# Kernel tuning notes

Measured on AMD Instinct MI355X. Metric: run time of the kernel, lower is better.

The kernel has to match this reference:

```python
import jax, jax.numpy as jnp
import numpy as np

BS = 4096
N_AGENTS = 8
INPUT_SHAPE = 256
H = 256
N_ACTIONS = 30


def setup_inputs() -> dict:
    key = jax.random.key(0)
    ks = jax.random.split(key, 10)
    return {
        "inputs": jax.random.normal(ks[0], (BS * N_AGENTS, INPUT_SHAPE), jnp.float32),
        "hidden_state": jax.random.normal(ks[1], (BS * N_AGENTS, H), jnp.float32),
        # hypernet-generated per-agent weights are relu outputs -> nonnegative
        "fc1_w": jax.random.uniform(ks[2], (N_AGENTS, INPUT_SHAPE, H), jnp.float32),
        "fc1_b": jax.random.uniform(ks[3], (N_AGENTS, H), jnp.float32),
        "rnn_ih_w": jax.random.uniform(ks[4], (N_AGENTS, H, 3 * H), jnp.float32),
        "rnn_ih_b": jax.random.uniform(ks[5], (N_AGENTS, 3 * H), jnp.float32),
        "rnn_hh_w": jax.random.uniform(ks[6], (N_AGENTS, H, 3 * H), jnp.float32),
        "rnn_hh_b": jax.random.uniform(ks[7], (N_AGENTS, 3 * H), jnp.float32),
        "fc2_w": jax.random.uniform(ks[8], (N_AGENTS, H, N_ACTIONS), jnp.float32),
        "fc2_b": jax.random.uniform(ks[9], (N_AGENTS, N_ACTIONS), jnp.float32),
    }


def reference(inputs, hidden_state, fc1_w, fc1_b, rnn_ih_w, rnn_ih_b,
              rnn_hh_w, rnn_hh_b, fc2_w, fc2_b):
    A = fc1_w.shape[0]
    inp = inputs.reshape(-1, A, fc1_w.shape[1])        # [bs, A, in]
    h_in = hidden_state.reshape(-1, A, rnn_hh_w.shape[1])  # [bs, A, H]

    # per-agent fc1: x = relu(inp @ fc1_w + fc1_b)
    x = jax.nn.relu(jnp.einsum('bai,aih->bah', inp, fc1_w) + fc1_b)

    # GRU-cell gate pre-activations with per-agent weights
    gi = jnp.einsum('bah,ahk->bak', x, rnn_ih_w) + rnn_ih_b     # [bs, A, 3H]
    gh = jnp.einsum('bah,ahk->bak', h_in, rnn_hh_w) + rnn_hh_b  # [bs, A, 3H]
    i_r, i_i, i_n = jnp.split(gi, 3, axis=-1)
    h_r, h_i, h_n = jnp.split(gh, 3, axis=-1)

    resetgate = jax.nn.sigmoid(i_r + h_r)
    inputgate = jax.nn.sigmoid(i_i + h_i)
    newgate = jnp.tanh(i_n + resetgate * h_n)
    h = newgate + inputgate * (h_in - newgate)          # [bs, A, H]

    q = jax.nn.relu(jnp.einsum('bah,aho->bao', h, fc2_w) + fc2_b)  # [bs, A, n_actions]
    return q.reshape(-1, q.shape[-1]), h.reshape(-1, h.shape[-1])
```

## Files before the change

### kernel.cpp

```cpp
#include <hip/hip_runtime.h>


typedef __attribute__((ext_vector_type(4))) float f32x4;
typedef __attribute__((ext_vector_type(8))) short s8;
typedef __attribute__((ext_vector_type(4))) unsigned short us4;
typedef __attribute__((ext_vector_type(8))) unsigned short us8;

#define QSIZE   983040
#define W1H_OFF 0
#define W1L_OFF 524288
#define WIH_OFF 1048576
#define WHH_OFF 2621440
#define W2T_OFF 4194304
#define XB_OFF  4259840
#define HB_OFF  12648448
#define RSX_U   21037056
#define RSH_U   21102592
#define WS_NEED_NEW 42336256ull

static __device__ __forceinline__ unsigned short f2bf(float f) {
  union { float f; unsigned u; } v; v.f = f;
  unsigned r = v.u + 0x7FFFu + ((v.u >> 16) & 1u);
  return (unsigned short)(r >> 16);
}
static __device__ __forceinline__ float bf2f(unsigned short u) {
  union { unsigned u; float f; } v; v.u = ((unsigned)u) << 16;
  return v.f;
}
static __device__ __forceinline__ float sigm(float x) {
  return 1.0f / (1.0f + __expf(-x));
}
static __device__ __forceinline__ float tanh_(float x) {
  return 1.0f - 2.0f / (__expf(2.0f * x) + 1.0f);
}

__global__ void prep_weights(const float* __restrict__ fc1w,
                             const float* __restrict__ rihw,
                             const float* __restrict__ rhhw,
                             const float* __restrict__ fc2w,
                             unsigned short* __restrict__ ws) {
  int q = blockIdx.x * 256 + threadIdx.x;
  if (q < 131072) {
    int a = q >> 14, rem = q & 16383;
    int cb = rem >> 10, s = rem & 1023;
    int ks = s >> 7, l4 = (s >> 5) & 3, l16 = (s >> 1) & 15, hf = s & 1;
    int n = cb * 16 + l16, k0 = ks * 32 + l4 * 8 + hf * 4;
    const float* sp = fc1w + a * 65536 + k0 * 256 + n;
    float v0 = sp[0], v1 = sp[256], v2 = sp[512], v3 = sp[768];
    us4 hi = { f2bf(v0), f2bf(v1), f2bf(v2), f2bf(v3) };
    us4 lo = { f2bf(v0 - bf2f(hi[0])), f2bf(v1 - bf2f(hi[1])),
               f2bf(v2 - bf2f(hi[2])), f2bf(v3 - bf2f(hi[3])) };
    int o = a * 65536 + cb * 4096 + ks * 512 + l4 * 128 + l16 * 8 + hf * 4;
    *(us4*)(ws + W1H_OFF + o) = hi;
    *(us4*)(ws + W1L_OFF + o) = lo;
  } else if (q < 524288) {
    int t = q - 131072;
    int a = t / 49152, rem = t % 49152;
    int cb = rem >> 10, s = rem & 1023;
    int ks = s >> 7, l4 = (s >> 5) & 3, l16 = (s >> 1) & 15, hf = s & 1;
    int n = cb * 16 + l16, k0 = ks * 32 + l4 * 8 + hf * 4;
    const float* sp = rihw + a * 196608 + k0 * 768 + n;
    us4 v = { f2bf(sp[0] - 0.5f), f2bf(sp[768] - 0.5f),
              f2bf(sp[1536] - 0.5f), f2bf(sp[2304] - 0.5f) };
    *(us4*)(ws + WIH_OFF + a * 196608 + cb * 4096 + ks * 512 + l4 * 128
            + l16 * 8 + hf * 4) = v;
  } else if (q < 917504) {
    int t = q - 524288;
    int a = t / 49152, rem = t % 49152;
    int cb = rem >> 10, s = rem & 1023;
    int ks = s >> 7, l4 = (s >> 5) & 3, l16 = (s >> 1) & 15, hf = s & 1;
    int n = cb * 16 + l16, k0 = ks * 32 + l4 * 8 + hf * 4;
    const float* sp = rhhw + a * 196608 + k0 * 768 + n;
    us4 v = { f2bf(sp[0] - 0.5f), f2bf(sp[768] - 0.5f),
              f2bf(sp[1536] - 0.5f), f2bf(sp[2304] - 0.5f) };
    *(us4*)(ws + WHH_OFF + a * 196608 + cb * 4096 + ks * 512 + l4 * 128
            + l16 * 8 + hf * 4) = v;
  } else if (q < 933888) {
    int t = q - 917504;
    int a = t >> 11, rem = t & 2047;
    int cb = rem >> 10, s = rem & 1023;
    int ks = s >> 7, l4 = (s >> 5) & 3, l16 = (s >> 1) & 15, hf = s & 1;
    int n = cb * 16 + l16, k0 = ks * 32 + l4 * 8 + hf * 4;
    us4 v = { 0, 0, 0, 0 };
    if (n < 30) {
      const float* sp = fc2w + a * 7680 + k0 * 30 + n;
      v = (us4){ f2bf(sp[0]), f2bf(sp[30]), f2bf(sp[60]), f2bf(sp[90]) };
    }
    *(us4*)(ws + W2T_OFF + a * 8192 + cb * 4096 + ks * 512 + l4 * 128
            + l16 * 8 + hf * 4) = v;
  }
}

static __device__ __forceinline__ void stage_split(unsigned short* p0,
                                                   unsigned short* p1,
                                                   const float* __restrict__ src,
                                                   int rowbase, int a, int tid) {
#pragma unroll
  for (int k = 0; k < 8; ++k) {
    int j = tid + k * 256;
    int r = j >> 6;
    int c4 = (j & 63) << 2;
    const float* p = src + ((((rowbase + r) << 3) + a) << 8) + c4;
    float4 v = *(const float4*)p;
    us4 hi = { f2bf(v.x), f2bf(v.y), f2bf(v.z), f2bf(v.w) };
    us4 lo = { f2bf(v.x - bf2f(hi[0])), f2bf(v.y - bf2f(hi[1])),
               f2bf(v.z - bf2f(hi[2])), f2bf(v.w - bf2f(hi[3])) };
    int idx = ((r << 8) + c4) ^ ((r & 7) << 3);
    *(us4*)(p0 + idx) = hi;
    *(us4*)(p1 + idx) = lo;
  }
}

static __device__ __forceinline__ void stage_single(unsigned short* p,
                                                    const float* __restrict__ src,
                                                    int rowbase, int a, int tid) {
#pragma unroll
  for (int k = 0; k < 8; ++k) {
    int j = tid + k * 256;
    int r = j >> 6;
    int c4 = (j & 63) << 2;
    const float* sp = src + ((((rowbase + r) << 3) + a) << 8) + c4;
    float4 v = *(const float4*)sp;
    us4 hi = { f2bf(v.x), f2bf(v.y), f2bf(v.z), f2bf(v.w) };
    int idx = ((r << 8) + c4) ^ ((r & 7) << 3);
    *(us4*)(p + idx) = hi;
  }
}

static __device__ __forceinline__ void mma64f(const unsigned short* lds,
                                              const unsigned short* __restrict__ wf,
                                              int cb0, int lane, int l16, int l4,
                                              f32x4 (&acc)[2][4]) {
#pragma unroll
  for (int ks = 0; ks < 8; ++ks) {
    s8 af[2], bw[4];
#pragma unroll
    for (int mt = 0; mt < 2; ++mt) {
      int row = mt * 16 + l16;
      int idx = ((row << 8) + ks * 32 + 8 * l4) ^ ((row & 7) << 3);
      af[mt] = *(const s8*)(lds + idx);
    }
#pragma unroll
    for (int nt = 0; nt < 4; ++nt)
      bw[nt] = *(const s8*)(wf + (cb0 + nt) * 4096 + ks * 512 + lane * 8);
#pragma unroll
    for (int mt = 0; mt < 2; ++mt)
#pragma unroll
      for (int nt = 0; nt < 4; ++nt)
        acc[mt][nt] = __builtin_amdgcn_mfma_f32_16x16x32_bf16(
            af[mt], bw[nt], acc[mt][nt], 0, 0, 0);
  }
}

static __device__ __forceinline__ void mma16f(const unsigned short* lds,
                                              const unsigned short* __restrict__ wf,
                                              int cb, int lane, int l16, int l4,
                                              f32x4 (&acc)[2]) {
#pragma unroll
  for (int ks = 0; ks < 8; ++ks) {
    s8 bw = *(const s8*)(wf + cb * 4096 + ks * 512 + lane * 8);
#pragma unroll
    for (int mt = 0; mt < 2; ++mt) {
      int row = mt * 16 + l16;
      int idx = ((row << 8) + ks * 32 + 8 * l4) ^ ((row & 7) << 3);
      s8 af = *(const s8*)(lds + idx);
      acc[mt] = __builtin_amdgcn_mfma_f32_16x16x32_bf16(af, bw, acc[mt], 0, 0, 0);
    }
  }
}

__global__ __launch_bounds__(256, 2) void k1_fc1(
    const float* __restrict__ inp, const float* __restrict__ hin,
    const float* __restrict__ b1, unsigned short* __restrict__ ws) {
  __shared__ __align__(16) unsigned short P0[32 * 256];
  __shared__ __align__(16) unsigned short P1[32 * 256];
  __shared__ float RSXP[8][32], RSHP[8][32];
  const int tid = threadIdx.x;
  const int a = blockIdx.x & 7;
  const int rt = blockIdx.x >> 3;
  const int rowbase = rt * 32;
  const int lane = tid & 63, w = tid >> 6;
  const int l16 = lane & 15, l4 = lane >> 4;
  const int n0 = w * 64;

  stage_split(P0, P1, inp, rowbase, a, tid);
  __syncthreads();

  f32x4 XA[2][4];
#pragma unroll
  for (int mt = 0; mt < 2; ++mt)
#pragma unroll
    for (int nt = 0; nt < 4; ++nt) XA[mt][nt] = (f32x4){0.f, 0.f, 0.f, 0.f};
  mma64f(P0, ws + W1H_OFF + a * 65536, w * 4, lane, l16, l4, XA);
  mma64f(P1, ws + W1H_OFF + a * 65536, w * 4, lane, l16, l4, XA);
  mma64f(P0, ws + W1L_OFF + a * 65536, w * 4, lane, l16, l4, XA);
  __syncthreads();

#pragma unroll
  for (int nt = 0; nt < 4; ++nt) {
    int col = n0 + nt * 16 + l16;
    float bb = b1[a * 256 + col];
#pragma unroll
    for (int mt = 0; mt < 2; ++mt)
#pragma unroll
      for (int r = 0; r < 4; ++r) {
        float v = fmaxf(XA[mt][nt][r] + bb, 0.f);
        int row = mt * 16 + l4 * 4 + r;
        P0[((row << 8) + col) ^ ((row & 7) << 3)] = f2bf(v);
      }
  }
  stage_single(P1, hin, rowbase, a, tid);
  __syncthreads();

  const int rbg = (a << 8) + rt * 2;
#pragma unroll
  for (int i = 0; i < 4; ++i) {
    int c = tid + i * 256;
    int rb = c >> 9, s = c & 511;
    int row = rb * 16 + (s & 15);
    int col = ((s >> 6) << 5) + (((s >> 4) & 3) << 3);
    int idx = ((row << 8) + col) ^ ((row & 7) << 3);
    *(us8*)(ws + XB_OFF + (rbg + rb) * 4096 + s * 8) = *(const us8*)(P0 + idx);
    *(us8*)(ws + HB_OFF + (rbg + rb) * 4096 + s * 8) = *(const us8*)(P1 + idx);
  }

  {
    int row = tid >> 3, qd = tid & 7;
    float sx = 0.f, sh = 0.f;
#pragma unroll
    for (int i = 0; i < 8; ++i) {
      int c = qd * 32 + i * 4;
      int idx = ((row << 8) + c) ^ ((row & 7) << 3);
      us4 vx = *(const us4*)(P0 + idx);
      us4 vh = *(const us4*)(P1 + idx);
      sx += bf2f(vx[0]) + bf2f(vx[1]) + bf2f(vx[2]) + bf2f(vx[3]);
      sh += bf2f(vh[0]) + bf2f(vh[1]) + bf2f(vh[2]) + bf2f(vh[3]);
    }
    RSXP[qd][row] = sx; RSHP[qd][row] = sh;
  }
  __syncthreads();
  if (tid < 32) {
    float sx = 0.f, sh = 0.f;
#pragma unroll
    for (int qd = 0; qd < 8; ++qd) { sx += RSXP[qd][tid]; sh += RSHP[qd][tid]; }
    float* rsxg = (float*)(ws + RSX_U);
    float* rshg = (float*)(ws + RSH_U);
    rsxg[a * 4096 + rowbase + tid] = sx;
    rshg[a * 4096 + rowbase + tid] = sh;
  }
}

__global__ __launch_bounds__(256, 2) void k2_gates_nw(
    const float* __restrict__ hin, const float* __restrict__ bih,
    const float* __restrict__ bhh, const unsigned short* __restrict__ ws,
    float* __restrict__ out) {
  __shared__ __align__(16) unsigned short AX[2 * 4096];
  __shared__ __align__(16) unsigned short AH[2 * 4096];
  const int tid  = threadIdx.x;
  const int lane = tid & 63;
  const int w    = tid >> 6;
  const int bid  = blockIdx.x;
  const int a    = bid & 7;
  const int g    = bid >> 3;
  const int rt   = g >> 1;
  const int cs   = (g & 1) * 4 + w;
  const int rowbase = rt * 32;
  const int n0   = cs * 32;
  const int l16  = lane & 15, l4 = lane >> 4;

  {
    const unsigned short* XFg = ws + XB_OFF + ((a << 8) + rt * 2) * 4096;
    const unsigned short* HFg = ws + HB_OFF + ((a << 8) + rt * 2) * 4096;
#pragma unroll
    for (int i = 0; i < 4; ++i) {
      int c = tid + i * 256;
      *(us8*)(AX + c * 8) = *(const us8*)(XFg + c * 8);
      *(us8*)(AH + c * 8) = *(const us8*)(HFg + c * 8);
    }
  }
  __syncthreads();

  const unsigned short* WihR = ws + WIH_OFF + a * 196608 + (cs * 2) * 4096 + lane * 8;
  const unsigned short* WhhR = ws + WHH_OFF + a * 196608 + (cs * 2) * 4096 + lane * 8;

  f32x4 R[2][2], I[2][2], T[2][2], G[2][2];
#pragma unroll
  for (int mt = 0; mt < 2; ++mt)
#pragma unroll
    for (int nt = 0; nt < 2; ++nt) {
      R[mt][nt] = (f32x4){0.f, 0.f, 0.f, 0.f};
      I[mt][nt] = (f32x4){0.f, 0.f, 0.f, 0.f};
      T[mt][nt] = (f32x4){0.f, 0.f, 0.f, 0.f};
      G[mt][nt] = (f32x4){0.f, 0.f, 0.f, 0.f};
    }

#pragma unroll 2
  for (int ks = 0; ks < 8; ++ks) {
    const int ko = ks * 512 + lane * 8;
    s8 ax[2], ah[2];
#pragma unroll
    for (int mt = 0; mt < 2; ++mt) {
      ax[mt] = *(const s8*)(AX + mt * 4096 + ko);
      ah[mt] = *(const s8*)(AH + mt * 4096 + ko);
    }
    const int kg = ks * 512;
    s8 bxr[2], bhr[2], bxi[2], bhi[2], bxn[2], bhn[2];
#pragma unroll
    for (int nt = 0; nt < 2; ++nt) {
      bxr[nt] = *(const s8*)(WihR + nt * 4096 + kg);
      bhr[nt] = *(const s8*)(WhhR + nt * 4096 + kg);
      bxi[nt] = *(const s8*)(WihR + (16 + nt) * 4096 + kg);
      bhi[nt] = *(const s8*)(WhhR + (16 + nt) * 4096 + kg);
      bxn[nt] = *(const s8*)(WihR + (32 + nt) * 4096 + kg);
      bhn[nt] = *(const s8*)(WhhR + (32 + nt) * 4096 + kg);
    }
#pragma unroll
    for (int mt = 0; mt < 2; ++mt)
#pragma unroll
      for (int nt = 0; nt < 2; ++nt) {
        R[mt][nt] = __builtin_amdgcn_mfma_f32_16x16x32_bf16(ax[mt], bxr[nt], R[mt][nt], 0, 0, 0);
        R[mt][nt] = __builtin_amdgcn_mfma_f32_16x16x32_bf16(ah[mt], bhr[nt], R[mt][nt], 0, 0, 0);
        I[mt][nt] = __builtin_amdgcn_mfma_f32_16x16x32_bf16(ax[mt], bxi[nt], I[mt][nt], 0, 0, 0);
        I[mt][nt] = __builtin_amdgcn_mfma_f32_16x16x32_bf16(ah[mt], bhi[nt], I[mt][nt], 0, 0, 0);
        G[mt][nt] = __builtin_amdgcn_mfma_f32_16x16x32_bf16(ax[mt], bxn[nt], G[mt][nt], 0, 0, 0);
        T[mt][nt] = __builtin_amdgcn_mfma_f32_16x16x32_bf16(ah[mt], bhn[nt], T[mt][nt], 0, 0, 0);
      }
  }

  const float* rsxg = (const float*)(ws + RSX_U) + a * 4096 + rowbase;
  const float* rshg = (const float*)(ws + RSH_U) + a * 4096 + rowbase;
#pragma unroll
  for (int mt = 0; mt < 2; ++mt) {
    float4 sx4 = *(const float4*)(rsxg + mt * 16 + l4 * 4);
    float4 sh4 = *(const float4*)(rshg + mt * 16 + l4 * 4);
    float rsx[4] = { sx4.x, sx4.y, sx4.z, sx4.w };
    float rsh[4] = { sh4.x, sh4.y, sh4.z, sh4.w };
#pragma unroll
    for (int nt = 0; nt < 2; ++nt) {
      int col = n0 + nt * 16 + l16;
      float br = bih[a * 768 + col] + bhh[a * 768 + col];
      float bi = bih[a * 768 + 256 + col] + bhh[a * 768 + 256 + col];
      float bnh = bhh[a * 768 + 512 + col];
      float bni = bih[a * 768 + 512 + col];
#pragma unroll
      for (int r = 0; r < 4; ++r) {
        float rg = sigm(R[mt][nt][r] + 0.5f * (rsx[r] + rsh[r]) + br);
        float t  = rg * (T[mt][nt][r] + 0.5f * rsh[r] + bnh);
        float ng = tanh_(G[mt][nt][r] + 0.5f * rsx[r] + bni + t);
        float ig = sigm(I[mt][nt][r] + 0.5f * (rsx[r] + rsh[r]) + bi);
        int row = mt * 16 + l4 * 4 + r;
        int flat = ((rowbase + row) << 3) + a;
        float hv = hin[(flat << 8) + col];
        out[QSIZE + (flat << 8) + col] = ng + ig * (hv - ng);
      }
    }
  }
}

__global__ __launch_bounds__(128) void k3_fc2(
    const float* __restrict__ b2, const unsigned short* __restrict__ ws,
    float* __restrict__ out) {
  __shared__ __align__(16) unsigned short HB[32 * 256];
  const int tid = threadIdx.x;
  const int a = blockIdx.x & 7;
  const int rowbase = (blockIdx.x >> 3) * 32;
  const int lane = tid & 63, w = tid >> 6;
  const int l16 = lane & 15, l4 = lane >> 4;

#pragma unroll
  for (int k = 0; k < 16; ++k) {
    int j = tid + k * 128;
    int r = j >> 6;
    int c4 = (j & 63) << 2;
    const float* sp = out + QSIZE + ((((rowbase + r) << 3) + a) << 8) + c4;
    float4 v = *(const float4*)sp;
    us4 hi = { f2bf(v.x), f2bf(v.y), f2bf(v.z), f2bf(v.w) };
    int idx = ((r << 8) + c4) ^ ((r & 7) << 3);
    *(us4*)(HB + idx) = hi;
  }
  __syncthreads();

  f32x4 qa[2];
  qa[0] = (f32x4){0.f, 0.f, 0.f, 0.f};
  qa[1] = (f32x4){0.f, 0.f, 0.f, 0.f};
#pragma unroll
  for (int ks = 0; ks < 8; ++ks) {
    int row = w * 16 + l16;
    int idx = ((row << 8) + ks * 32 + 8 * l4) ^ ((row & 7) << 3);
    s8 af = *(const s8*)(HB + idx);
#pragma unroll
    for (int nt = 0; nt < 2; ++nt) {
      s8 bw = *(const s8*)(ws + W2T_OFF + a * 8192 + nt * 4096 + ks * 512 + lane * 8);
      qa[nt] = __builtin_amdgcn_mfma_f32_16x16x32_bf16(af, bw, qa[nt], 0, 0, 0);
    }
  }
#pragma unroll
  for (int nt = 0; nt < 2; ++nt) {
    int col = nt * 16 + l16;
    if (col < 30) {
      float bb = b2[a * 30 + col];
#pragma unroll
      for (int r = 0; r < 4; ++r) {
        int row = w * 16 + l4 * 4 + r;
        out[(((rowbase + row) << 3) + a) * 30 + col] = fmaxf(qa[nt][r] + bb, 0.f);
      }
    }
  }
}

__global__ __launch_bounds__(256, 2) void fused_agent_rnn(
    const float* __restrict__ inp,  const float* __restrict__ hin,
    const float* __restrict__ b1,   const float* __restrict__ bih,
    const float* __restrict__ bhh,  const float* __restrict__ b2,
    const unsigned short* __restrict__ ws, float* __restrict__ out) {
  __shared__ __align__(16) unsigned short P0[32 * 256];
  __shared__ __align__(16) unsigned short P1[32 * 256];
  __shared__ float RSXP[8][32], RSHP[8][32];
  __shared__ float RSX[32], RSH[32];

  const int tid = threadIdx.x;
  const int a = blockIdx.x & 7;
  const int rowbase = (blockIdx.x >> 3) * 32;
  const int lane = tid & 63, w = tid >> 6;
  const int l16 = lane & 15, l4 = lane >> 4;
  const int n0 = w * 64;

  stage_split(P0, P1, inp, rowbase, a, tid);
  __syncthreads();
  {
    f32x4 XA[2][4];
#pragma unroll
    for (int mt = 0; mt < 2; ++mt)
#pragma unroll
      for (int nt = 0; nt < 4; ++nt) XA[mt][nt] = (f32x4){0.f, 0.f, 0.f, 0.f};
    mma64f(P0, ws + W1H_OFF + a * 65536, w * 4, lane, l16, l4, XA);
    mma64f(P1, ws + W1H_OFF + a * 65536, w * 4, lane, l16, l4, XA);
    mma64f(P0, ws + W1L_OFF + a * 65536, w * 4, lane, l16, l4, XA);
    __syncthreads();
#pragma unroll
    for (int nt = 0; nt < 4; ++nt) {
      int col = n0 + nt * 16 + l16;
      float bb = b1[a * 256 + col];
#pragma unroll
      for (int mt = 0; mt < 2; ++mt)
#pragma unroll
        for (int r = 0; r < 4; ++r) {
          float v = fmaxf(XA[mt][nt][r] + bb, 0.f);
          int row = mt * 16 + l4 * 4 + r;
          P0[((row << 8) + col) ^ ((row & 7) << 3)] = f2bf(v);
        }
    }
  }
  stage_single(P1, hin, rowbase, a, tid);
  __syncthreads();
  {
    int row = tid >> 3, qd = tid & 7;
    float sx = 0.f, sh = 0.f;
#pragma unroll
    for (int i = 0; i < 8; ++i) {
      int c = qd * 32 + i * 4;
      int idx = ((row << 8) + c) ^ ((row & 7) << 3);
      us4 vx = *(const us4*)(P0 + idx);
      us4 vh = *(const us4*)(P1 + idx);
      sx += bf2f(vx[0]) + bf2f(vx[1]) + bf2f(vx[2]) + bf2f(vx[3]);
      sh += bf2f(vh[0]) + bf2f(vh[1]) + bf2f(vh[2]) + bf2f(vh[3]);
    }
    RSXP[qd][row] = sx; RSHP[qd][row] = sh;
  }
  __syncthreads();
  if (tid < 32) {
    float sx = 0.f, sh = 0.f;
#pragma unroll
    for (int qd = 0; qd < 8; ++qd) { sx += RSXP[qd][tid]; sh += RSHP[qd][tid]; }
    RSX[tid] = sx; RSH[tid] = sh;
  }
  __syncthreads();

  const unsigned short* WihF = ws + WIH_OFF + a * 196608;
  const unsigned short* WhhF = ws + WHH_OFF + a * 196608;

  for (int nt = 0; nt < 4; ++nt) {
    const int col = n0 + nt * 16 + l16;
    const int cb = w * 4 + nt;
    f32x4 R4[2], T4[2], G4[2];
#pragma unroll
    for (int mt = 0; mt < 2; ++mt) R4[mt] = (f32x4){0.f, 0.f, 0.f, 0.f};
    mma16f(P0, WihF, cb, lane, l16, l4, R4);
    mma16f(P1, WhhF, cb, lane, l16, l4, R4);
    {
      float bb = bih[a * 768 + col] + bhh[a * 768 + col];
#pragma unroll
      for (int mt = 0; mt < 2; ++mt)
#pragma unroll
        for (int r = 0; r < 4; ++r) {
          int row = mt * 16 + l4 * 4 + r;
          R4[mt][r] = sigm(R4[mt][r] + 0.5f * (RSX[row] + RSH[row]) + bb);
        }
    }
#pragma unroll
    for (int mt = 0; mt < 2; ++mt) T4[mt] = (f32x4){0.f, 0.f, 0.f, 0.f};
    mma16f(P1, WhhF, 32 + cb, lane, l16, l4, T4);
    {
      float bb = bhh[a * 768 + 512 + col];
#pragma unroll
      for (int mt = 0; mt < 2; ++mt)
#pragma unroll
        for (int r = 0; r < 4; ++r) {
          int row = mt * 16 + l4 * 4 + r;
          T4[mt][r] = R4[mt][r] * (T4[mt][r] + 0.5f * RSH[row] + bb);
        }
    }
#pragma unroll
    for (int mt = 0; mt < 2; ++mt) G4[mt] = (f32x4){0.f, 0.f, 0.f, 0.f};
    mma16f(P0, WihF, 32 + cb, lane, l16, l4, G4);
    {
      float bb = bih[a * 768 + 512 + col];
#pragma unroll
      for (int mt = 0; mt < 2; ++mt)
#pragma unroll
        for (int r = 0; r < 4; ++r) {
          int row = mt * 16 + l4 * 4 + r;
          T4[mt][r] = tanh_(G4[mt][r] + 0.5f * RSX[row] + bb + T4[mt][r]);
        }
    }
#pragma unroll
    for (int mt = 0; mt < 2; ++mt) G4[mt] = (f32x4){0.f, 0.f, 0.f, 0.f};
    mma16f(P0, WihF, 16 + cb, lane, l16, l4, G4);
    mma16f(P1, WhhF, 16 + cb, lane, l16, l4, G4);
    {
      float bb = bih[a * 768 + 256 + col] + bhh[a * 768 + 256 + col];
#pragma unroll
      for (int mt = 0; mt < 2; ++mt)
#pragma unroll
        for (int r = 0; r < 4; ++r) {
          int row = mt * 16 + l4 * 4 + r;
          float ig = sigm(G4[mt][r] + 0.5f * (RSX[row] + RSH[row]) + bb);
          float hv = bf2f(P1[((row << 8) + col) ^ ((row & 7) << 3)]);
          float ng = T4[mt][r];
          out[QSIZE + ((((rowbase + row) << 3) + a) << 8) + col]
              = ng + ig * (hv - ng);
        }
    }
  }
  __syncthreads();
  stage_single(P0, out + QSIZE, rowbase, a, tid);
  __syncthreads();
  if (w < 2) {
    f32x4 qa[2];
    qa[0] = (f32x4){0.f, 0.f, 0.f, 0.f};
    qa[1] = (f32x4){0.f, 0.f, 0.f, 0.f};
#pragma unroll
    for (int ks = 0; ks < 8; ++ks) {
      int row = w * 16 + l16;
      int idx = ((row << 8) + ks * 32 + 8 * l4) ^ ((row & 7) << 3);
      s8 af = *(const s8*)(P0 + idx);
#pragma unroll
      for (int nt = 0; nt < 2; ++nt) {
        s8 bw = *(const s8*)(ws + W2T_OFF + a * 8192 + nt * 4096 + ks * 512 + lane * 8);
        qa[nt] = __builtin_amdgcn_mfma_f32_16x16x32_bf16(af, bw, qa[nt], 0, 0, 0);
      }
    }
#pragma unroll
    for (int nt = 0; nt < 2; ++nt) {
      int col = nt * 16 + l16;
      if (col < 30) {
        float bb = b2[a * 30 + col];
#pragma unroll
        for (int r = 0; r < 4; ++r) {
          int row = w * 16 + l4 * 4 + r;
          out[(((rowbase + row) << 3) + a) * 30 + col] = fmaxf(qa[nt][r] + bb, 0.f);
        }
      }
    }
  }
}

extern "C" void kernel_launch(void* const* d_in, const int* in_sizes, int n_in,
                              void* d_out, int out_size, void* d_ws, size_t ws_size,
                              hipStream_t stream) {
  const float* inputs = (const float*)d_in[0];
  const float* hidden = (const float*)d_in[1];
  const float* fc1w   = (const float*)d_in[2];
  const float* fc1b   = (const float*)d_in[3];
  const float* rihw   = (const float*)d_in[4];
  const float* rihb   = (const float*)d_in[5];
  const float* rhhw   = (const float*)d_in[6];
  const float* rhhb   = (const float*)d_in[7];
  const float* fc2w   = (const float*)d_in[8];
  const float* fc2b   = (const float*)d_in[9];
  unsigned short* ws  = (unsigned short*)d_ws;
  float* out          = (float*)d_out;

  hipLaunchKernelGGL(prep_weights, dim3(3648), dim3(256), 0, stream,
                     fc1w, rihw, rhhw, fc2w, ws);

  if (ws_size >= WS_NEED_NEW) {
    hipLaunchKernelGGL(k1_fc1, dim3(1024), dim3(256), 0, stream,
                       inputs, hidden, fc1b, ws);
    hipLaunchKernelGGL(k2_gates_nw, dim3(2048), dim3(256), 0, stream,
                       hidden, rihb, rhhb, ws, out);
    hipLaunchKernelGGL(k3_fc2, dim3(1024), dim3(128), 0, stream, fc2b, ws, out);
  } else {
    hipLaunchKernelGGL(fused_agent_rnn, dim3(1024), dim3(256), 0, stream,
                       inputs, hidden, fc1b, rihb, rhhb, fc2b, ws, out);
  }
}
```

Before: 103.7 us.

## Fuse GRU gate and fc2 kernels, reuse staged hidden state, interleave fc1 MFMAs

Merges the gate kernel and the fc2 kernel into one 512-thread block per 32-row tile. The new hidden state is written to shared memory as bf16 and consumed directly by the fc2 MMA, which removes the fp32 re-read of h from global memory and one kernel launch. h_in is now read from the bf16 staged tile in LDS instead of global fp32, which lowers the precision of the h_in term in the update. fc1's three MMA passes are interleaved into a single k-loop so A fragments are reused, at the cost of higher register pressure.

New measurement: 95.15 us. 8.3% less time.

```diff
diff --git a/kernel.cpp b/kernel.cpp
--- a/kernel.cpp
+++ b/kernel.cpp
@@ -191,9 +191,36 @@
   for (int mt = 0; mt < 2; ++mt)
 #pragma unroll
     for (int nt = 0; nt < 4; ++nt) XA[mt][nt] = (f32x4){0.f, 0.f, 0.f, 0.f};
-  mma64f(P0, ws + W1H_OFF + a * 65536, w * 4, lane, l16, l4, XA);
-  mma64f(P1, ws + W1H_OFF + a * 65536, w * 4, lane, l16, l4, XA);
-  mma64f(P0, ws + W1L_OFF + a * 65536, w * 4, lane, l16, l4, XA);
+
+  {
+    const unsigned short* WH = ws + W1H_OFF + a * 65536 + (w * 4) * 4096 + lane * 8;
+    const unsigned short* WL = ws + W1L_OFF + a * 65536 + (w * 4) * 4096 + lane * 8;
+#pragma unroll 2
+    for (int ks = 0; ks < 8; ++ks) {
+      s8 af0[2], af1[2];
+#pragma unroll
+      for (int mt = 0; mt < 2; ++mt) {
+        int row = mt * 16 + l16;
+        int idx = ((row << 8) + ks * 32 + 8 * l4) ^ ((row & 7) << 3);
+        af0[mt] = *(const s8*)(P0 + idx);
+        af1[mt] = *(const s8*)(P1 + idx);
+      }
+      s8 bh[4], bl[4];
+#pragma unroll
+      for (int nt = 0; nt < 4; ++nt) {
+        bh[nt] = *(const s8*)(WH + nt * 4096 + ks * 512);
+        bl[nt] = *(const s8*)(WL + nt * 4096 + ks * 512);
+      }
+#pragma unroll
+      for (int mt = 0; mt < 2; ++mt)
+#pragma unroll
+        for (int nt = 0; nt < 4; ++nt) {
+          XA[mt][nt] = __builtin_amdgcn_mfma_f32_16x16x32_bf16(af0[mt], bh[nt], XA[mt][nt], 0, 0, 0);
+          XA[mt][nt] = __builtin_amdgcn_mfma_f32_16x16x32_bf16(af1[mt], bh[nt], XA[mt][nt], 0, 0, 0);
+          XA[mt][nt] = __builtin_amdgcn_mfma_f32_16x16x32_bf16(af0[mt], bl[nt], XA[mt][nt], 0, 0, 0);
+        }
+    }
+  }
   __syncthreads();
 
 #pragma unroll
@@ -250,30 +277,28 @@
   }
 }
 
-__global__ __launch_bounds__(256, 2) void k2_gates_nw(
-    const float* __restrict__ hin, const float* __restrict__ bih,
-    const float* __restrict__ bhh, const unsigned short* __restrict__ ws,
+__global__ __launch_bounds__(512, 3) void k2_fused(
+    const float* __restrict__ bih, const float* __restrict__ bhh,
+    const float* __restrict__ b2, const unsigned short* __restrict__ ws,
     float* __restrict__ out) {
-  __shared__ __align__(16) unsigned short AX[2 * 4096];
-  __shared__ __align__(16) unsigned short AH[2 * 4096];
+  __shared__ __align__(16) unsigned short AX[8192];
+  __shared__ __align__(16) unsigned short AH[8192];
   const int tid  = threadIdx.x;
   const int lane = tid & 63;
   const int w    = tid >> 6;
-  const int bid  = blockIdx.x;
-  const int a    = bid & 7;
-  const int g    = bid >> 3;
-  const int rt   = g >> 1;
-  const int cs   = (g & 1) * 4 + w;
+  const int a    = blockIdx.x & 7;
+  const int rt   = blockIdx.x >> 3;
   const int rowbase = rt * 32;
+  const int cs   = w;
   const int n0   = cs * 32;
-  const int l16  = lane & 15, l4 = lane >> 4;
+  const int l16  = lane & 15, qr = lane >> 4;
 
   {
     const unsigned short* XFg = ws + XB_OFF + ((a << 8) + rt * 2) * 4096;
     const unsigned short* HFg = ws + HB_OFF + ((a << 8) + rt * 2) * 4096;
 #pragma unroll
-    for (int i = 0; i < 4; ++i) {
-      int c = tid + i * 256;
+    for (int i = 0; i < 2; ++i) {
+      int c = tid + i * 512;
       *(us8*)(AX + c * 8) = *(const us8*)(XFg + c * 8);
       *(us8*)(AH + c * 8) = *(const us8*)(HFg + c * 8);
     }
@@ -329,10 +354,11 @@
 
   const float* rsxg = (const float*)(ws + RSX_U) + a * 4096 + rowbase;
   const float* rshg = (const float*)(ws + RSH_U) + a * 4096 + rowbase;
+  float hloc[2][2][4];
 #pragma unroll
   for (int mt = 0; mt < 2; ++mt) {
-    float4 sx4 = *(const float4*)(rsxg + mt * 16 + l4 * 4);
-    float4 sh4 = *(const float4*)(rshg + mt * 16 + l4 * 4);
+    float4 sx4 = *(const float4*)(rsxg + mt * 16 + qr * 4);
+    float4 sh4 = *(const float4*)(rshg + mt * 16 + qr * 4);
     float rsx[4] = { sx4.x, sx4.y, sx4.z, sx4.w };
     float rsh[4] = { sh4.x, sh4.y, sh4.z, sh4.w };
 #pragma unroll
@@ -348,61 +374,56 @@
         float t  = rg * (T[mt][nt][r] + 0.5f * rsh[r] + bnh);
         float ng = tanh_(G[mt][nt][r] + 0.5f * rsx[r] + bni + t);
         float ig = sigm(I[mt][nt][r] + 0.5f * (rsx[r] + rsh[r]) + bi);
-        int row = mt * 16 + l4 * 4 + r;
+        int row = mt * 16 + qr * 4 + r;
         int flat = ((rowbase + row) << 3) + a;
-        float hv = hin[(flat << 8) + col];
-        out[QSIZE + (flat << 8) + col] = ng + ig * (hv - ng);
-      }
-    }
-  }
-}
-
-__global__ __launch_bounds__(128) void k3_fc2(
-    const float* __restrict__ b2, const unsigned short* __restrict__ ws,
-    float* __restrict__ out) {
-  __shared__ __align__(16) unsigned short HB[32 * 256];
-  const int tid = threadIdx.x;
-  const int a = blockIdx.x & 7;
-  const int rowbase = (blockIdx.x >> 3) * 32;
-  const int lane = tid & 63, w = tid >> 6;
-  const int l16 = lane & 15, l4 = lane >> 4;
-
-#pragma unroll
-  for (int k = 0; k < 16; ++k) {
-    int j = tid + k * 128;
-    int r = j >> 6;
-    int c4 = (j & 63) << 2;
-    const float* sp = out + QSIZE + ((((rowbase + r) << 3) + a) << 8) + c4;
-    float4 v = *(const float4*)sp;
-    us4 hi = { f2bf(v.x), f2bf(v.y), f2bf(v.z), f2bf(v.w) };
-    int idx = ((r << 8) + c4) ^ ((r & 7) << 3);
-    *(us4*)(HB + idx) = hi;
-  }
-  __syncthreads();
-
-  f32x4 qa[2];
-  qa[0] = (f32x4){0.f, 0.f, 0.f, 0.f};
-  qa[1] = (f32x4){0.f, 0.f, 0.f, 0.f};
-#pragma unroll
-  for (int ks = 0; ks < 8; ++ks) {
-    int row = w * 16 + l16;
-    int idx = ((row << 8) + ks * 32 + 8 * l4) ^ ((row & 7) << 3);
-    s8 af = *(const s8*)(HB + idx);
+        int hidx = mt * 4096 + cs * 512 + (nt * 2 + (l16 >> 3)) * 128
+                 + (qr * 4 + r) * 8 + (l16 & 7);
+        float hv = bf2f(AH[hidx]);
+        float h = ng + ig * (hv - ng);
+        out[QSIZE + (flat << 8) + col] = h;
+        hloc[mt][nt][r] = h;
+      }
+    }
+  }
+  __syncthreads();
+
+#pragma unroll
+  for (int mt = 0; mt < 2; ++mt)
+#pragma unroll
+    for (int nt = 0; nt < 2; ++nt)
+#pragma unroll
+      for (int r = 0; r < 4; ++r) {
+        int row = mt * 16 + qr * 4 + r;
+        int col = n0 + nt * 16 + l16;
+        AX[((row << 8) + col) ^ ((row & 7) << 3)] = f2bf(hloc[mt][nt][r]);
+      }
+  __syncthreads();
+
+  if (w < 2) {
+    f32x4 qa[2];
+    qa[0] = (f32x4){0.f, 0.f, 0.f, 0.f};
+    qa[1] = (f32x4){0.f, 0.f, 0.f, 0.f};
+#pragma unroll
+    for (int ks = 0; ks < 8; ++ks) {
+      int row = w * 16 + l16;
+      int idx = ((row << 8) + ks * 32 + 8 * qr) ^ ((row & 7) << 3);
+      s8 af = *(const s8*)(AX + idx);
+#pragma unroll
+      for (int nt = 0; nt < 2; ++nt) {
+        s8 bw = *(const s8*)(ws + W2T_OFF + a * 8192 + nt * 4096 + ks * 512 + lane * 8);
+        qa[nt] = __builtin_amdgcn_mfma_f32_16x16x32_bf16(af, bw, qa[nt], 0, 0, 0);
+      }
+    }
 #pragma unroll
     for (int nt = 0; nt < 2; ++nt) {
-      s8 bw = *(const s8*)(ws + W2T_OFF + a * 8192 + nt * 4096 + ks * 512 + lane * 8);
-      qa[nt] = __builtin_amdgcn_mfma_f32_16x16x32_bf16(af, bw, qa[nt], 0, 0, 0);
-    }
-  }
-#pragma unroll
-  for (int nt = 0; nt < 2; ++nt) {
-    int col = nt * 16 + l16;
-    if (col < 30) {
-      float bb = b2[a * 30 + col];
-#pragma unroll
-      for (int r = 0; r < 4; ++r) {
-        int row = w * 16 + l4 * 4 + r;
-        out[(((rowbase + row) << 3) + a) * 30 + col] = fmaxf(qa[nt][r] + bb, 0.f);
+      int col = nt * 16 + l16;
+      if (col < 30) {
+        float bb = b2[a * 30 + col];
+#pragma unroll
+        for (int r = 0; r < 4; ++r) {
+          int row = w * 16 + qr * 4 + r;
+          out[(((rowbase + row) << 3) + a) * 30 + col] = fmaxf(qa[nt][r] + bb, 0.f);
+        }
       }
     }
   }
@@ -597,9 +618,8 @@
   if (ws_size >= WS_NEED_NEW) {
     hipLaunchKernelGGL(k1_fc1, dim3(1024), dim3(256), 0, stream,
                        inputs, hidden, fc1b, ws);
-    hipLaunchKernelGGL(k2_gates_nw, dim3(2048), dim3(256), 0, stream,
-                       hidden, rihb, rhhb, ws, out);
-    hipLaunchKernelGGL(k3_fc2, dim3(1024), dim3(128), 0, stream, fc2b, ws, out);
+    hipLaunchKernelGGL(k2_fused, dim3(1024), dim3(512), 0, stream,
+                       rihb, rhhb, fc2b, ws, out);
   } else {
     hipLaunchKernelGGL(fused_agent_rnn, dim3(1024), dim3(256), 0, stream,
                        inputs, hidden, fc1b, rihb, rhhb, fc2b, ws, out);
```
